# Optimization experiments

Measured on AMD Instinct MI355X. Metric: run time of the kernel, lower is better.

The kernel has to match this reference:

```python
import jax, jax.numpy as jnp
import numpy as np

B, L, E, H = 2, 2048, 1024, 16
D = E // H

def setup_inputs() -> dict:
    key = jax.random.key(0)
    ks = jax.random.split(key, 6)
    s = 1.0 / np.sqrt(E)
    return {
        "x": jax.random.normal(ks[0], (B, L, E), dtype=jnp.float32),
        "attention_mask": jnp.ones((B, L), dtype=jnp.float32),
        "Wq": jax.random.normal(ks[1], (E, E), dtype=jnp.float32) * s,
        "Wk": jax.random.normal(ks[2], (E, E), dtype=jnp.float32) * s,
        "Wv": jax.random.normal(ks[3], (E, E), dtype=jnp.float32) * s,
        "Wo": jax.random.normal(ks[4], (E, E), dtype=jnp.float32) * s,
        "bo": jnp.zeros((E,), dtype=jnp.float32),
    }

def reference(x, attention_mask, Wq, Wk, Wv, Wo, bo):
    b, l, e = x.shape
    h, d = H, D

    def proj(W):
        # (B,L,E) @ (E,E)^T -> (B,L,E) -> (B,H,L,D)
        return (x @ W.T).reshape(b, l, h, d).transpose(0, 2, 1, 3)

    q, k, v = proj(Wq), proj(Wk), proj(Wv)

    # multiplicative attention mask on q, k, v (mask shape (B,L) -> (B,1,L,1))
    m = attention_mask[:, None, :, None].astype(x.dtype)
    q, k, v = q * m, k * m, v * m

    scale = 1.0 / np.sqrt(d)
    scores = jnp.einsum('bhqd,bhkd->bhqk', q, k) * scale  # (B,H,L,L)
    causal = jnp.tril(jnp.ones((l, l), dtype=bool))
    scores = jnp.where(causal[None, None], scores, -jnp.inf)
    attn = jax.nn.softmax(scores, axis=-1)
    y = jnp.einsum('bhqk,bhkd->bhqd', attn, v)  # (B,H,L,D)
    y = y.transpose(0, 2, 1, 3).reshape(b, l, e)
    return y @ Wo.T + bo
```

## Files before the change

kernel.cpp:

```cpp
#include <hip/hip_runtime.h>
#include <cstdint>
#include <cstddef>
#include <math.h>

#define BB 2
#define LL 2048
#define EE 1024
#define HH 16
#define DD 64
#define MM (BB*LL)

typedef short short8 __attribute__((ext_vector_type(8)));
typedef float f32x4 __attribute__((ext_vector_type(4)));
typedef float f32x16 __attribute__((ext_vector_type(16)));

#define GPTR __attribute__((address_space(1)))
#define LPTR __attribute__((address_space(3)))

__device__ __forceinline__ unsigned short f32_bf16(float f) {
  union { float f; unsigned u; } c; c.f = f;
  c.u += 0x7fffu + ((c.u >> 16) & 1u);
  return (unsigned short)(c.u >> 16);
}

__device__ __forceinline__ unsigned pk_bf16(float lo, float hi) {
  unsigned r;
  asm("v_cvt_pk_bf16_f32 %0, %1, %2" : "=v"(r) : "v"(lo), "v"(hi));
  return r;
}
__device__ __forceinline__ void swap32(unsigned &a, unsigned &b) {
  asm("v_permlane32_swap_b32 %0, %1" : "+v"(a), "+v"(b));
}
__device__ __forceinline__ f32x16 zero16() {
  f32x16 v;
  #pragma unroll
  for (int e = 0; e < 16; ++e) v[e] = 0.f;
  return v;
}

__global__ void cvt_all(const float* __restrict__ x,  const float* __restrict__ wq,
                        const float* __restrict__ wk, const float* __restrict__ wv,
                        const float* __restrict__ wo,
                        unsigned short* __restrict__ xb,  unsigned short* __restrict__ wqb,
                        unsigned short* __restrict__ wkb, unsigned short* __restrict__ wvb,
                        unsigned short* __restrict__ wob)
{
  int i = (blockIdx.x * 256 + threadIdx.x) * 4;
  if (i >= MM * EE + 4 * EE * EE) return;
  const float* s; unsigned short* d; int off;
  if (i < MM * EE) { s = x; d = xb; off = i; }
  else {
    int k = i - MM * EE;
    int w = k >> 20;
    off = k & (EE * EE - 1);
    s = (w == 0) ? wq : (w == 1) ? wk : (w == 2) ? wv : wo;
    d = (w == 0) ? wqb : (w == 1) ? wkb : (w == 2) ? wvb : wob;
  }
  float4 v = *(const float4*)(s + off);
  union { unsigned short s[4]; uint2 u; } o;
  o.s[0] = f32_bf16(v.x); o.s[1] = f32_bf16(v.y);
  o.s[2] = f32_bf16(v.z); o.s[3] = f32_bf16(v.w);
  *(uint2*)(d + off) = o.u;
}

template<int MODE>
__global__ __launch_bounds__(256, 2)
void gemm128(const unsigned short* __restrict__ A,
             const unsigned short* __restrict__ W0,
             const unsigned short* __restrict__ W1,
             const unsigned short* __restrict__ W2,
             const float* __restrict__ mask,
             const float* __restrict__ bias,
             unsigned short* __restrict__ O0,
             unsigned short* __restrict__ O1,
             unsigned short* __restrict__ O2,
             float* __restrict__ OF)
{
  constexpr int K = EE;
  const int tid = threadIdx.x;
  const int lane = tid & 63;
  const int wid = tid >> 6;
  const int g = lane >> 4, li = lane & 15;
  const int m0 = blockIdx.y * 128;
  const int n0 = blockIdx.x * 128;
  const int z = blockIdx.z;

  const unsigned short* Wp = W0;
  if (MODE == 0) Wp = (z == 0) ? W0 : ((z == 1) ? W1 : W2);

  __shared__ unsigned short As[128 * 64];
  __shared__ unsigned short Bs[128 * 64];

  f32x4 acc[4][4];
  f32x4 zero = {0.f, 0.f, 0.f, 0.f};
  #pragma unroll
  for (int i = 0; i < 4; ++i)
    #pragma unroll
    for (int j = 0; j < 4; ++j) acc[i][j] = zero;

  const int wm = (wid >> 1) * 64;
  const int wn = (wid & 1) * 64;

  for (int kt = 0; kt < K; kt += 64) {
    #pragma unroll
    for (int j = 0; j < 4; ++j) {
      int c = j * 256 + tid;
      int row = c >> 3;
      int lcol = ((c & 7) * 16) ^ ((row & 7) << 4);
      __builtin_amdgcn_global_load_lds(
        (const GPTR void*)((const char*)(A + (size_t)(m0 + row) * K + kt) + lcol),
        (LPTR void*)((char*)As + c * 16), 16, 0, 0);
      __builtin_amdgcn_global_load_lds(
        (const GPTR void*)((const char*)(Wp + (size_t)(n0 + row) * K + kt) + lcol),
        (LPTR void*)((char*)Bs + c * 16), 16, 0, 0);
    }
    __syncthreads();

    #pragma unroll
    for (int kk = 0; kk < 2; ++kk) {
      short8 a[4], b[4];
      const int colb = (kk * 32 + g * 8) * 2;
      #pragma unroll
      for (int i = 0; i < 4; ++i) {
        int ar = wm + i * 16 + li;
        a[i] = *(const short8*)((const char*)As + ar * 128 + (colb ^ ((ar & 7) << 4)));
        int br = wn + i * 16 + li;
        b[i] = *(const short8*)((const char*)Bs + br * 128 + (colb ^ ((br & 7) << 4)));
      }
      #pragma unroll
      for (int i = 0; i < 4; ++i)
        #pragma unroll
        for (int j = 0; j < 4; ++j)
          acc[i][j] = __builtin_amdgcn_mfma_f32_16x16x32_bf16(a[i], b[j], acc[i][j], 0, 0, 0);
    }
    __syncthreads();
  }

  if (MODE == 0) {
    if (z == 2) {
      #pragma unroll
      for (int i = 0; i < 4; ++i) {
        int mbase = m0 + wm + i * 16 + g * 4;
        int bb2 = mbase >> 11;
        int l0  = mbase & (LL - 1);
        float mk[4];
        #pragma unroll
        for (int r = 0; r < 4; ++r) mk[r] = mask[mbase + r];
        #pragma unroll
        for (int j = 0; j < 4; ++j) {
          int n = n0 + wn + j * 16 + li;
          int h2 = n >> 6, dd2 = n & 63;
          union { unsigned short s[4]; uint2 u; } o;
          #pragma unroll
          for (int r = 0; r < 4; ++r) o.s[r] = f32_bf16(acc[i][j][r] * mk[r]);
          *(uint2*)(O2 + ((size_t)(bb2 * HH + h2) * DD + dd2) * LL + l0) = o.u;
        }
      }
    } else {
      unsigned short* Op = (z == 0) ? O0 : O1;
      const float sc = (z == 0) ? 0.125f * 1.44269504088896f : 1.0f;
      #pragma unroll
      for (int i = 0; i < 4; ++i) {
        #pragma unroll
        for (int r = 0; r < 4; ++r) {
          int m = m0 + wm + i * 16 + g * 4 + r;
          float mk = mask[m] * sc;
          int bb = m >> 11;
          int l  = m & (LL - 1);
          #pragma unroll
          for (int j = 0; j < 4; ++j) {
            int n = n0 + wn + j * 16 + li;
            int h = n >> 6, d = n & 63;
            size_t off = (((size_t)(bb * HH + h)) * LL + l) * DD + d;
            Op[off] = f32_bf16(acc[i][j][r] * mk);
          }
        }
      }
    }
  } else {
    #pragma unroll
    for (int i = 0; i < 4; ++i) {
      #pragma unroll
      for (int j = 0; j < 4; ++j) {
        int n = n0 + wn + j * 16 + li;
        float bv = bias[n];
        #pragma unroll
        for (int r = 0; r < 4; ++r) {
          int m = m0 + wm + i * 16 + g * 4 + r;
          OF[(size_t)m * EE + n] = acc[i][j][r] + bv;
        }
      }
    }
  }
}

__global__ __launch_bounds__(128, 2)
void attn2(const unsigned short* __restrict__ Q,
           const unsigned short* __restrict__ K,
           const unsigned short* __restrict__ VT,
           unsigned short* __restrict__ Y)
{
  const int tid = threadIdx.x, lane = tid & 63, wq = tid >> 6;
  const int l31 = lane & 31, hi = lane >> 5;

  const int id = blockIdx.x;
  const int bh_lo = id & 7;
  const int r_ = id >> 3;
  const int bh = (r_ & 3) * 8 + bh_lo;
  const int qt = 31 - (r_ >> 2);
  const int q0 = qt * 64;
  const int b = bh >> 4, h = bh & (HH - 1);
  const size_t kbase = (size_t)bh * LL * DD;

  __shared__ unsigned short Ks[2][64 * 64];
  __shared__ unsigned short Vs[2][64 * 64];

  const unsigned short* Kg  = K + kbase;
  const unsigned short* VTg = VT + kbase;

  const int qrow = q0 + wq * 32 + l31;
  const int qmin = q0 + wq * 32;

  short8 qf[4];
  {
    const unsigned short* Qr = Q + kbase + (size_t)qrow * DD + hi * 8;
    #pragma unroll
    for (int kc = 0; kc < 4; ++kc) qf[kc] = *(const short8*)(Qr + kc * 16);
  }

  f32x16 ot0 = zero16(), ot1 = zero16();
  float m = -INFINITY, lsum = 0.f;

  const int nt = qt + 1;

  auto stage = [&](int buf, int t2) {
    const int kv0s = t2 << 6;
    #pragma unroll
    for (int u = 0; u < 4; ++u) {
      int c = u * 128 + tid;
      int row = c >> 3;
      int cb = (c & 7) * 16;
      int scol = cb ^ ((row & 7) << 4);
      __builtin_amdgcn_global_load_lds(
        (const GPTR void*)((const char*)(Kg + (size_t)(kv0s + row) * DD) + scol),
        (LPTR void*)((char*)Ks[buf] + c * 16), 16, 0, 0);
      __builtin_amdgcn_global_load_lds(
        (const GPTR void*)((const char*)(VTg + (size_t)row * LL + kv0s) + scol),
        (LPTR void*)((char*)Vs[buf] + c * 16), 16, 0, 0);
    }
  };

  stage(0, 0);
  int cur = 0;

  const int cb0 = hi * 16;
  const int r0 = l31, r1 = 32 + l31;
  const int swz = ((l31 & 7) << 4);

  for (int t = 0; t < nt; ++t) {
    __syncthreads();
    const char* Kb_ = (const char*)Ks[cur];
    const char* Vb_ = (const char*)Vs[cur];

    short8 k0[4], k1[4], v0[4], v1[4];
    #pragma unroll
    for (int kc = 0; kc < 4; ++kc) {
      int cb = (kc * 32 + cb0) ^ swz;
      k0[kc] = *(const short8*)(Kb_ + r0 * 128 + cb);
      k1[kc] = *(const short8*)(Kb_ + r1 * 128 + cb);
      v0[kc] = *(const short8*)(Vb_ + r0 * 128 + cb);
      v1[kc] = *(const short8*)(Vb_ + r1 * 128 + cb);
    }
    if (t + 1 < nt) stage(cur ^ 1, t + 1);
    __builtin_amdgcn_sched_barrier(0);

    const int kv0 = t << 6;
    const bool need1 = (kv0 + 32 <= qmin + 31);

    f32x16 s0 = zero16(), s1 = zero16();
    __builtin_amdgcn_s_setprio(1);
    if (need1) {
      #pragma unroll
      for (int kc = 0; kc < 4; ++kc) {
        s0 = __builtin_amdgcn_mfma_f32_32x32x16_bf16(k0[kc], qf[kc], s0, 0, 0, 0);
        s1 = __builtin_amdgcn_mfma_f32_32x32x16_bf16(k1[kc], qf[kc], s1, 0, 0, 0);
      }
    } else {
      #pragma unroll
      for (int kc = 0; kc < 4; ++kc)
        s0 = __builtin_amdgcn_mfma_f32_32x32x16_bf16(k0[kc], qf[kc], s0, 0, 0, 0);
    }
    __builtin_amdgcn_s_setprio(0);

    if (kv0 + 63 > qmin) {
      #pragma unroll
      for (int rg = 0; rg < 4; ++rg)
        #pragma unroll
        for (int e = 0; e < 4; ++e) {
          int kvg = kv0 + rg * 8 + hi * 4 + e;
          if (kvg > qrow)                s0[rg * 4 + e] = -INFINITY;
          if (need1 && kvg + 32 > qrow)  s1[rg * 4 + e] = -INFINITY;
        }
    }

    float red[16];
    #pragma unroll
    for (int e = 0; e < 16; ++e) red[e] = need1 ? fmaxf(s0[e], s1[e]) : s0[e];
    #pragma unroll
    for (int st = 8; st >= 1; st >>= 1)
      #pragma unroll
      for (int e = 0; e < 8; ++e) if (e < st) red[e] = fmaxf(red[e], red[e + st]);
    float mv = red[0];
    mv = fmaxf(mv, __shfl_xor(mv, 32, 64));

    if (!__all(mv <= m + 8.0f)) {
      float mnew = fmaxf(m, mv);
      float al = exp2f(m - mnew);
      m = mnew;
      lsum *= al;
      #pragma unroll
      for (int e = 0; e < 16; ++e) { ot0[e] *= al; ot1[e] *= al; }
    }

    float rs;
    {
      float ra[16];
      #pragma unroll
      for (int e = 0; e < 16; ++e) { s0[e] = exp2f(s0[e] - m); ra[e] = s0[e]; }
      if (need1) {
        #pragma unroll
        for (int e = 0; e < 16; ++e) { s1[e] = exp2f(s1[e] - m); ra[e] += s1[e]; }
      }
      #pragma unroll
      for (int st = 8; st >= 1; st >>= 1)
        #pragma unroll
        for (int e = 0; e < 8; ++e) if (e < st) ra[e] += ra[e + st];
      rs = ra[0];
    }
    rs += __shfl_xor(rs, 32, 64);
    lsum += rs;

    auto mkfrag = [&](const f32x16& sv, int base) -> short8 {
      unsigned a0 = pk_bf16(sv[base + 0], sv[base + 1]);
      unsigned a1 = pk_bf16(sv[base + 2], sv[base + 3]);
      unsigned b0 = pk_bf16(sv[base + 4], sv[base + 5]);
      unsigned b1 = pk_bf16(sv[base + 6], sv[base + 7]);
      swap32(a0, b0);
      swap32(a1, b1);
      union { unsigned u[4]; short8 s; } f;
      f.u[0] = a0; f.u[1] = a1; f.u[2] = b0; f.u[3] = b1;
      return f.s;
    };
    short8 pf[4];
    pf[0] = mkfrag(s0, 0); pf[1] = mkfrag(s0, 8);
    if (need1) { pf[2] = mkfrag(s1, 0); pf[3] = mkfrag(s1, 8); }

    __builtin_amdgcn_s_setprio(1);
    if (need1) {
      #pragma unroll
      for (int kc = 0; kc < 4; ++kc) {
        ot0 = __builtin_amdgcn_mfma_f32_32x32x16_bf16(v0[kc], pf[kc], ot0, 0, 0, 0);
        ot1 = __builtin_amdgcn_mfma_f32_32x32x16_bf16(v1[kc], pf[kc], ot1, 0, 0, 0);
      }
    } else {
      #pragma unroll
      for (int kc = 0; kc < 2; ++kc) {
        ot0 = __builtin_amdgcn_mfma_f32_32x32x16_bf16(v0[kc], pf[kc], ot0, 0, 0, 0);
        ot1 = __builtin_amdgcn_mfma_f32_32x32x16_bf16(v1[kc], pf[kc], ot1, 0, 0, 0);
      }
    }
    __builtin_amdgcn_s_setprio(0);
    cur ^= 1;
  }

  float inv = 1.0f / lsum;
  unsigned short* Yr = Y + ((size_t)b * LL + qrow) * EE + h * DD;
  #pragma unroll
  for (int rg = 0; rg < 4; ++rg) {
    union { unsigned short s[4]; uint2 u; } o0, o1;
    #pragma unroll
    for (int e = 0; e < 4; ++e) {
      o0.s[e] = f32_bf16(ot0[rg * 4 + e] * inv);
      o1.s[e] = f32_bf16(ot1[rg * 4 + e] * inv);
    }
    *(uint2*)(Yr + rg * 8 + hi * 4) = o0.u;
    *(uint2*)(Yr + 32 + rg * 8 + hi * 4) = o1.u;
  }
}

extern "C" void kernel_launch(void* const* d_in, const int* in_sizes, int n_in,
                              void* d_out, int out_size, void* d_ws, size_t ws_size,
                              hipStream_t stream) {
  const float* x    = (const float*)d_in[0];
  const float* mask = (const float*)d_in[1];
  const float* Wq   = (const float*)d_in[2];
  const float* Wk   = (const float*)d_in[3];
  const float* Wv   = (const float*)d_in[4];
  const float* Wo   = (const float*)d_in[5];
  const float* bo   = (const float*)d_in[6];
  float* out = (float*)d_out;

  char* ws = (char*)d_ws;
  unsigned short* xb  = (unsigned short*)(ws);
  unsigned short* wqb = (unsigned short*)(ws + ((size_t)8  << 20));
  unsigned short* wkb = (unsigned short*)(ws + ((size_t)10 << 20));
  unsigned short* wvb = (unsigned short*)(ws + ((size_t)12 << 20));
  unsigned short* wob = (unsigned short*)(ws + ((size_t)14 << 20));
  unsigned short* Qb  = (unsigned short*)(ws + ((size_t)16 << 20));
  unsigned short* Kb  = (unsigned short*)(ws + ((size_t)24 << 20));
  unsigned short* VTb = (unsigned short*)(ws + ((size_t)32 << 20));
  unsigned short* Yb  = (unsigned short*)(ws + ((size_t)40 << 20));

  cvt_all<<<8192, 256, 0, stream>>>(x, Wq, Wk, Wv, Wo, xb, wqb, wkb, wvb, wob);

  gemm128<0><<<dim3(EE / 128, MM / 128, 3), 256, 0, stream>>>(
      xb, wqb, wkb, wvb, mask, nullptr, Qb, Kb, VTb, nullptr);

  attn2<<<dim3(1024), 128, 0, stream>>>(Qb, Kb, VTb, Yb);

  gemm128<1><<<dim3(EE / 128, MM / 128, 1), 256, 0, stream>>>(
      Yb, wob, nullptr, nullptr, nullptr, bo, nullptr, nullptr, nullptr, out);
}
```

Before: 130.0 us.

## Rewrite attention as single-wave blocks loading K/V directly into registers

Replaces the two-wave attention kernel, which staged K and V through shared memory, with a one-wave-per-block kernel. Each block handles 32 query rows and reads K and V tiles straight from global memory into registers, double-buffered across iterations. Causal masking is applied only on the last tile, and the cross-half reductions use permlane32 swaps instead of shuffles. This removes LDS traffic and block barriers and doubles the block count for finer causal load balance, at the cost of uncoalesced global reads, no K/V reuse between waves, and more register pressure.

Result: slower. 138.8 us (+6.7%).

```diff
diff --git a/kernel.cpp b/kernel.cpp
--- a/kernel.cpp
+++ b/kernel.cpp
@@ -30,6 +30,20 @@
 }
 __device__ __forceinline__ void swap32(unsigned &a, unsigned &b) {
   asm("v_permlane32_swap_b32 %0, %1" : "+v"(a), "+v"(b));
+}
+__device__ __forceinline__ float xh_max(float v) {
+  union { float f; unsigned u; } a, b;
+  a.f = v;
+  asm("v_mov_b32 %0, %1" : "=&v"(b.u) : "v"(a.u));
+  asm("v_permlane32_swap_b32 %0, %1" : "+v"(a.u), "+v"(b.u));
+  return fmaxf(a.f, b.f);
+}
+__device__ __forceinline__ float xh_sum(float v) {
+  union { float f; unsigned u; } a, b;
+  a.f = v;
+  asm("v_mov_b32 %0, %1" : "=&v"(b.u) : "v"(a.u));
+  asm("v_permlane32_swap_b32 %0, %1" : "+v"(a.u), "+v"(b.u));
+  return a.f + b.f;
 }
 __device__ __forceinline__ f32x16 zero16() {
   f32x16 v;
@@ -194,32 +208,29 @@
   }
 }
 
-__global__ __launch_bounds__(128, 2)
-void attn2(const unsigned short* __restrict__ Q,
+__global__ __launch_bounds__(64, 2)
+void attn3(const unsigned short* __restrict__ Q,
            const unsigned short* __restrict__ K,
            const unsigned short* __restrict__ VT,
            unsigned short* __restrict__ Y)
 {
-  const int tid = threadIdx.x, lane = tid & 63, wq = tid >> 6;
+  const int lane = threadIdx.x;
   const int l31 = lane & 31, hi = lane >> 5;
 
   const int id = blockIdx.x;
-  const int bh_lo = id & 7;
+  const int lo = id & 7;
   const int r_ = id >> 3;
-  const int bh = (r_ & 3) * 8 + bh_lo;
-  const int qt = 31 - (r_ >> 2);
-  const int q0 = qt * 64;
+  const int bh = (r_ & 3) * 8 + lo;
+  const int qt = 63 - (r_ >> 2);
+  const int q0 = qt * 32;
   const int b = bh >> 4, h = bh & (HH - 1);
   const size_t kbase = (size_t)bh * LL * DD;
 
-  __shared__ unsigned short Ks[2][64 * 64];
-  __shared__ unsigned short Vs[2][64 * 64];
-
   const unsigned short* Kg  = K + kbase;
   const unsigned short* VTg = VT + kbase;
 
-  const int qrow = q0 + wq * 32 + l31;
-  const int qmin = q0 + wq * 32;
+  const int qrow = q0 + l31;
+  const int nt = qt + 1;
 
   short8 qf[4];
   {
@@ -231,87 +242,56 @@
   f32x16 ot0 = zero16(), ot1 = zero16();
   float m = -INFINITY, lsum = 0.f;
 
-  const int nt = qt + 1;
-
-  auto stage = [&](int buf, int t2) {
-    const int kv0s = t2 << 6;
-    #pragma unroll
-    for (int u = 0; u < 4; ++u) {
-      int c = u * 128 + tid;
-      int row = c >> 3;
-      int cb = (c & 7) * 16;
-      int scol = cb ^ ((row & 7) << 4);
-      __builtin_amdgcn_global_load_lds(
-        (const GPTR void*)((const char*)(Kg + (size_t)(kv0s + row) * DD) + scol),
-        (LPTR void*)((char*)Ks[buf] + c * 16), 16, 0, 0);
-      __builtin_amdgcn_global_load_lds(
-        (const GPTR void*)((const char*)(VTg + (size_t)row * LL + kv0s) + scol),
-        (LPTR void*)((char*)Vs[buf] + c * 16), 16, 0, 0);
-    }
-  };
-
-  stage(0, 0);
-  int cur = 0;
-
-  const int cb0 = hi * 16;
-  const int r0 = l31, r1 = 32 + l31;
-  const int swz = ((l31 & 7) << 4);
-
-  for (int t = 0; t < nt; ++t) {
-    __syncthreads();
-    const char* Kb_ = (const char*)Ks[cur];
-    const char* Vb_ = (const char*)Vs[cur];
-
-    short8 k0[4], k1[4], v0[4], v1[4];
-    #pragma unroll
-    for (int kc = 0; kc < 4; ++kc) {
-      int cb = (kc * 32 + cb0) ^ swz;
-      k0[kc] = *(const short8*)(Kb_ + r0 * 128 + cb);
-      k1[kc] = *(const short8*)(Kb_ + r1 * 128 + cb);
-      v0[kc] = *(const short8*)(Vb_ + r0 * 128 + cb);
-      v1[kc] = *(const short8*)(Vb_ + r1 * 128 + cb);
-    }
-    if (t + 1 < nt) stage(cur ^ 1, t + 1);
-    __builtin_amdgcn_sched_barrier(0);
-
-    const int kv0 = t << 6;
-    const bool need1 = (kv0 + 32 <= qmin + 31);
-
-    f32x16 s0 = zero16(), s1 = zero16();
+  short8 kA[4], vA[4], kB[4], vB[4];
+
+  {
+    const unsigned short* Kp = Kg + ((size_t)l31 << 6) + hi * 8;
+    #pragma unroll
+    for (int kc = 0; kc < 4; ++kc) kA[kc] = *(const short8*)(Kp + kc * 16);
+    const unsigned short* Vp = VTg + ((size_t)l31 << 11) + hi * 8;
+    vA[0] = *(const short8*)(Vp);
+    vA[1] = *(const short8*)(Vp + 16);
+    vA[2] = *(const short8*)(Vp + (32 << 11));
+    vA[3] = *(const short8*)(Vp + (32 << 11) + 16);
+  }
+
+  auto body = [&](short8 (&ck)[4], short8 (&cv)[4],
+                  short8 (&nk)[4], short8 (&nv)[4], int t) {
+    const int kv0 = t << 5;
+    if (t + 1 < nt) {
+      const unsigned short* Kp = Kg + ((size_t)(kv0 + 32 + l31) << 6) + hi * 8;
+      #pragma unroll
+      for (int kc = 0; kc < 4; ++kc) nk[kc] = *(const short8*)(Kp + kc * 16);
+      const unsigned short* Vp = VTg + ((size_t)l31 << 11) + kv0 + 32 + hi * 8;
+      nv[0] = *(const short8*)(Vp);
+      nv[1] = *(const short8*)(Vp + 16);
+      nv[2] = *(const short8*)(Vp + (32 << 11));
+      nv[3] = *(const short8*)(Vp + (32 << 11) + 16);
+    }
+
+    f32x16 s = zero16();
     __builtin_amdgcn_s_setprio(1);
-    if (need1) {
-      #pragma unroll
-      for (int kc = 0; kc < 4; ++kc) {
-        s0 = __builtin_amdgcn_mfma_f32_32x32x16_bf16(k0[kc], qf[kc], s0, 0, 0, 0);
-        s1 = __builtin_amdgcn_mfma_f32_32x32x16_bf16(k1[kc], qf[kc], s1, 0, 0, 0);
-      }
-    } else {
-      #pragma unroll
-      for (int kc = 0; kc < 4; ++kc)
-        s0 = __builtin_amdgcn_mfma_f32_32x32x16_bf16(k0[kc], qf[kc], s0, 0, 0, 0);
-    }
+    #pragma unroll
+    for (int kc = 0; kc < 4; ++kc)
+      s = __builtin_amdgcn_mfma_f32_32x32x16_bf16(ck[kc], qf[kc], s, 0, 0, 0);
     __builtin_amdgcn_s_setprio(0);
 
-    if (kv0 + 63 > qmin) {
-      #pragma unroll
-      for (int rg = 0; rg < 4; ++rg)
-        #pragma unroll
-        for (int e = 0; e < 4; ++e) {
-          int kvg = kv0 + rg * 8 + hi * 4 + e;
-          if (kvg > qrow)                s0[rg * 4 + e] = -INFINITY;
-          if (need1 && kvg + 32 > qrow)  s1[rg * 4 + e] = -INFINITY;
-        }
-    }
-
-    float red[16];
-    #pragma unroll
-    for (int e = 0; e < 16; ++e) red[e] = need1 ? fmaxf(s0[e], s1[e]) : s0[e];
-    #pragma unroll
-    for (int st = 8; st >= 1; st >>= 1)
-      #pragma unroll
-      for (int e = 0; e < 8; ++e) if (e < st) red[e] = fmaxf(red[e], red[e + st]);
-    float mv = red[0];
-    mv = fmaxf(mv, __shfl_xor(mv, 32, 64));
+    if (t == nt - 1) {
+      #pragma unroll
+      for (int i = 0; i < 16; ++i) {
+        int kvr = (i & 3) + 8 * (i >> 2) + 4 * hi;
+        if (kvr > l31) s[i] = -INFINITY;
+      }
+    }
+
+    float red[8];
+    #pragma unroll
+    for (int e = 0; e < 8; ++e) red[e] = fmaxf(s[e], s[e + 8]);
+    #pragma unroll
+    for (int st = 4; st >= 1; st >>= 1)
+      #pragma unroll
+      for (int e = 0; e < 4; ++e) if (e < st) red[e] = fmaxf(red[e], red[e + st]);
+    float mv = xh_max(red[0]);
 
     if (!__all(mv <= m + 8.0f)) {
       float mnew = fmaxf(m, mv);
@@ -322,55 +302,41 @@
       for (int e = 0; e < 16; ++e) { ot0[e] *= al; ot1[e] *= al; }
     }
 
-    float rs;
-    {
-      float ra[16];
-      #pragma unroll
-      for (int e = 0; e < 16; ++e) { s0[e] = exp2f(s0[e] - m); ra[e] = s0[e]; }
-      if (need1) {
-        #pragma unroll
-        for (int e = 0; e < 16; ++e) { s1[e] = exp2f(s1[e] - m); ra[e] += s1[e]; }
-      }
-      #pragma unroll
-      for (int st = 8; st >= 1; st >>= 1)
-        #pragma unroll
-        for (int e = 0; e < 8; ++e) if (e < st) ra[e] += ra[e + st];
-      rs = ra[0];
-    }
-    rs += __shfl_xor(rs, 32, 64);
-    lsum += rs;
-
-    auto mkfrag = [&](const f32x16& sv, int base) -> short8 {
-      unsigned a0 = pk_bf16(sv[base + 0], sv[base + 1]);
-      unsigned a1 = pk_bf16(sv[base + 2], sv[base + 3]);
-      unsigned b0 = pk_bf16(sv[base + 4], sv[base + 5]);
-      unsigned b1 = pk_bf16(sv[base + 6], sv[base + 7]);
+    float ra[8];
+    #pragma unroll
+    for (int e = 0; e < 16; ++e) s[e] = exp2f(s[e] - m);
+    #pragma unroll
+    for (int e = 0; e < 8; ++e) ra[e] = s[e] + s[e + 8];
+    #pragma unroll
+    for (int st = 4; st >= 1; st >>= 1)
+      #pragma unroll
+      for (int e = 0; e < 4; ++e) if (e < st) ra[e] += ra[e + st];
+    lsum += xh_sum(ra[0]);
+
+    auto mkfrag = [&](int base) -> short8 {
+      unsigned a0 = pk_bf16(s[base + 0], s[base + 1]);
+      unsigned a1 = pk_bf16(s[base + 2], s[base + 3]);
+      unsigned b0 = pk_bf16(s[base + 4], s[base + 5]);
+      unsigned b1 = pk_bf16(s[base + 6], s[base + 7]);
       swap32(a0, b0);
       swap32(a1, b1);
-      union { unsigned u[4]; short8 s; } f;
+      union { unsigned u[4]; short8 s8; } f;
       f.u[0] = a0; f.u[1] = a1; f.u[2] = b0; f.u[3] = b1;
-      return f.s;
+      return f.s8;
     };
-    short8 pf[4];
-    pf[0] = mkfrag(s0, 0); pf[1] = mkfrag(s0, 8);
-    if (need1) { pf[2] = mkfrag(s1, 0); pf[3] = mkfrag(s1, 8); }
+    short8 pf0 = mkfrag(0), pf1 = mkfrag(8);
 
     __builtin_amdgcn_s_setprio(1);
-    if (need1) {
-      #pragma unroll
-      for (int kc = 0; kc < 4; ++kc) {
-        ot0 = __builtin_amdgcn_mfma_f32_32x32x16_bf16(v0[kc], pf[kc], ot0, 0, 0, 0);
-        ot1 = __builtin_amdgcn_mfma_f32_32x32x16_bf16(v1[kc], pf[kc], ot1, 0, 0, 0);
-      }
-    } else {
-      #pragma unroll
-      for (int kc = 0; kc < 2; ++kc) {
-        ot0 = __builtin_amdgcn_mfma_f32_32x32x16_bf16(v0[kc], pf[kc], ot0, 0, 0, 0);
-        ot1 = __builtin_amdgcn_mfma_f32_32x32x16_bf16(v1[kc], pf[kc], ot1, 0, 0, 0);
-      }
-    }
+    ot0 = __builtin_amdgcn_mfma_f32_32x32x16_bf16(cv[0], pf0, ot0, 0, 0, 0);
+    ot0 = __builtin_amdgcn_mfma_f32_32x32x16_bf16(cv[1], pf1, ot0, 0, 0, 0);
+    ot1 = __builtin_amdgcn_mfma_f32_32x32x16_bf16(cv[2], pf0, ot1, 0, 0, 0);
+    ot1 = __builtin_amdgcn_mfma_f32_32x32x16_bf16(cv[3], pf1, ot1, 0, 0, 0);
     __builtin_amdgcn_s_setprio(0);
-    cur ^= 1;
+  };
+
+  for (int t = 0; t < nt; t += 2) {
+    body(kA, vA, kB, vB, t);
+    if (t + 1 < nt) body(kB, vB, kA, vA, t + 1);
   }
 
   float inv = 1.0f / lsum;
@@ -416,7 +382,7 @@
   gemm128<0><<<dim3(EE / 128, MM / 128, 3), 256, 0, stream>>>(
       xb, wqb, wkb, wvb, mask, nullptr, Qb, Kb, VTb, nullptr);
 
-  attn2<<<dim3(1024), 128, 0, stream>>>(Qb, Kb, VTb, Yb);
+  attn3<<<dim3(2048), 64, 0, stream>>>(Qb, Kb, VTb, Yb);
 
   gemm128<1><<<dim3(EE / 128, MM / 128, 1), 256, 0, stream>>>(
       Yb, wob, nullptr, nullptr, nullptr, bo, nullptr, nullptr, nullptr, out);
```
